# Performance work log

Hardware: AMD Instinct MI355X
Metric: run time of the kernel (lower is better)

The kernel has to match this reference:

```python
import jax, jax.numpy as jnp
import numpy as np

NUM_EXPERTS = 7
TRUNK_DIM = 64
HIDDEN = 64   # max(48, trunk_dim)
NUM_DEPTH_CLASSES = 3
BATCH = 262144


def setup_inputs() -> dict:
    key = jax.random.key(0)
    ks = jax.random.split(key, 8)
    trunk_feat = jax.random.normal(ks[0], (BATCH, TRUNK_DIM), dtype=jnp.float32)
    size_idx = jax.random.randint(ks[1], (BATCH,), 0, NUM_EXPERTS, dtype=jnp.int64)
    # Stacked expert MLP params: Linear(64,64) -> ReLU -> Linear(64,64) -> ReLU -> Linear(64,3)
    s1 = 1.0 / np.sqrt(TRUNK_DIM)
    s2 = 1.0 / np.sqrt(HIDDEN)
    W1 = jax.random.uniform(ks[2], (NUM_EXPERTS, TRUNK_DIM, HIDDEN), jnp.float32, -s1, s1)
    b1 = jax.random.uniform(ks[3], (NUM_EXPERTS, HIDDEN), jnp.float32, -s1, s1)
    W2 = jax.random.uniform(ks[4], (NUM_EXPERTS, HIDDEN, HIDDEN), jnp.float32, -s2, s2)
    b2 = jax.random.uniform(ks[5], (NUM_EXPERTS, HIDDEN), jnp.float32, -s2, s2)
    W3 = jax.random.uniform(ks[6], (NUM_EXPERTS, HIDDEN, NUM_DEPTH_CLASSES), jnp.float32, -s2, s2)
    b3 = jax.random.uniform(ks[7], (NUM_EXPERTS, NUM_DEPTH_CLASSES), jnp.float32, -s2, s2)
    return {"trunk_feat": trunk_feat, "size_idx": size_idx,
            "W1": W1, "b1": b1, "W2": W2, "b2": b2, "W3": W3, "b3": b3}


def _expert_mlp(x, W1, b1, W2, b2, W3, b3):
    # 3-layer MLP of one expert (dropout = identity in eval mode)
    h = jax.nn.relu(x @ W1 + b1)
    h = jax.nn.relu(h @ W2 + b2)
    return h @ W3 + b3  # [B, num_depth_classes]


def reference(trunk_feat, size_idx, W1, b1, W2, b2, W3, b3):
    # Hard routing (route_logits): rows with size_idx == e go through expert e;
    # expressed as masked accumulate so it is jit-friendly (no data-dependent shapes).
    B = trunk_feat.shape[0]
    logits = jnp.zeros((B, NUM_DEPTH_CLASSES), dtype=trunk_feat.dtype)
    for e in range(NUM_EXPERTS):  # fixed, small expert count
        le = _expert_mlp(trunk_feat, W1[e], b1[e], W2[e], b2[e], W3[e], b3[e])
        mask = (size_idx == e)[:, None]
        logits = logits + jnp.where(mask, le, jnp.zeros_like(le))
    probs = jax.nn.softmax(logits, axis=1)
    return logits, probs
```

## Files before the change

### kernel.cpp

```cpp
#include <hip/hip_runtime.h>
#include <stdint.h>

#define NE    7
#define DD    64
#define NDC   3
#define BLOCK 256
#define ROWS  256
#define NFRAG 18

typedef __fp16   half8 __attribute__((ext_vector_type(8)));
typedef float    f32x4 __attribute__((ext_vector_type(4)));
typedef uint32_t u32x4 __attribute__((ext_vector_type(4)));
typedef uint32_t u32x2 __attribute__((ext_vector_type(2)));
typedef __fp16   h2_t  __attribute__((ext_vector_type(2)));

__device__ __forceinline__ uint32_t pkrtz(float a, float b) {
  h2_t h = __builtin_amdgcn_cvt_pkrtz(a, b);
  return __builtin_bit_cast(uint32_t, h);
}
__device__ __forceinline__ f32x4 mfma16(u32x4 a, u32x4 b, f32x4 c) {
  return __builtin_amdgcn_mfma_f32_16x16x32_f16(
      __builtin_bit_cast(half8, a), __builtin_bit_cast(half8, b), c, 0, 0, 0);
}
__device__ __forceinline__ u32x4 relu_pack(f32x4 lo, f32x4 hi) {
  u32x4 t = { pkrtz(fmaxf(lo[0],0.f), fmaxf(lo[1],0.f)),
              pkrtz(fmaxf(lo[2],0.f), fmaxf(lo[3],0.f)),
              pkrtz(fmaxf(hi[0],0.f), fmaxf(hi[1],0.f)),
              pkrtz(fmaxf(hi[2],0.f), fmaxf(hi[3],0.f)) };
  return t;
}

__global__ __launch_bounds__(256) void pack_w2(
    const float* __restrict__ W1, const float* __restrict__ W2,
    const float* __restrict__ W3, uint32_t* __restrict__ ws) {
  __shared__ float wt[DD*DD];
  const int blk = blockIdx.x;
  const int e = blk >> 1, half = blk & 1;
  const float* Wsrc = (half ? W2 : W1) + (size_t)e*DD*DD;
  const float4* s4 = (const float4*)Wsrc;
  float4* d4 = (float4*)wt;
  #pragma unroll
  for (int i = 0; i < DD*DD/4/256; ++i)
    d4[i*256 + threadIdx.x] = s4[i*256 + threadIdx.x];
  __syncthreads();

  for (int idx = threadIdx.x; idx < 8*64; idx += 256) {
    const int fl = idx >> 6, l = idx & 63;
    const int nt = fl >> 1, ks = fl & 1;
    const int n  = nt*16 + (l & 15), g = l >> 4;
    uint32_t dst[4];
    #pragma unroll
    for (int d = 0; d < 4; ++d) {
      float v[2];
      #pragma unroll
      for (int h = 0; h < 2; ++h) {
        const int kk = 16*(d>>1) + 4*g + 2*(d&1) + h;
        v[h] = wt[(32*ks + kk)*DD + n];
      }
      dst[d] = pkrtz(v[0], v[1]);
    }
    uint32_t* p = ws + ((size_t)(e*NFRAG + half*8 + fl)*64 + l)*4;
    p[0]=dst[0]; p[1]=dst[1]; p[2]=dst[2]; p[3]=dst[3];
  }
  if (half == 0) {
    const float* Wl2 = W3 + (size_t)e*DD*NDC;
    for (int idx = threadIdx.x; idx < 2*64; idx += 256) {
      const int ks = idx >> 6, l = idx & 63;
      const int n  = l & 15, g = l >> 4;
      uint32_t dst[4];
      #pragma unroll
      for (int d = 0; d < 4; ++d) {
        float v[2];
        #pragma unroll
        for (int h = 0; h < 2; ++h) {
          const int kk = 16*(d>>1) + 4*g + 2*(d&1) + h;
          v[h] = (n < NDC) ? Wl2[(32*ks + kk)*NDC + n] : 0.0f;
        }
        dst[d] = pkrtz(v[0], v[1]);
      }
      uint32_t* p = ws + ((size_t)(e*NFRAG + 16 + ks)*64 + l)*4;
      p[0]=dst[0]; p[1]=dst[1]; p[2]=dst[2]; p[3]=dst[3];
    }
  }
}

__global__ __launch_bounds__(BLOCK, 3) void fused(
    const float* __restrict__ X, const int* __restrict__ S,
    const u32x4* __restrict__ wf,
    const float* __restrict__ b1, const float* __restrict__ b2,
    const float* __restrict__ b3,
    float* __restrict__ out, int B)
{
  __shared__ uint32_t pk[ROWS*32];
  __shared__ uint16_t srt[ROWS];
  __shared__ int wcnt[4][NE], woff[4][NE], cnt[NE];

  const int tid  = threadIdx.x;
  const int wv   = tid >> 6, lane = tid & 63;
  const int r15  = lane & 15, g = lane >> 4;
  const int base = blockIdx.x * ROWS;

  const int e_i = S[base + tid];

  u32x4 af[NFRAG];
  {
    const u32x4* wse = wf + (size_t)wv*NFRAG*64;
    #pragma unroll
    for (int f = 0; f < NFRAG; ++f) af[f] = wse[f*64 + lane];
  }

  {
    const float4* Xb = (const float4*)(X + (size_t)base * DD);
    #pragma unroll
    for (int it = 0; it < 16; ++it) {
      const int i = it*BLOCK + tid;
      const int r = i >> 4, q = i & 15;
      const float4 v = Xb[i];
      const int slotq = 4*(q >> 3) + (q & 3);
      const int hq    = (q >> 2) & 1;
      u32x2 w2 = { pkrtz(v.x, v.y), pkrtz(v.z, v.w) };
      *(u32x2*)&pk[r*32 + ((slotq ^ (r & 7)) << 2) + hq*2] = w2;
    }
  }

  int myprefix = 0;
  {
    unsigned long long mk[NE];
    #pragma unroll
    for (int q2 = 0; q2 < NE; ++q2) mk[q2] = __ballot(e_i == q2);
    #pragma unroll
    for (int q2 = 0; q2 < NE; ++q2)
      if (e_i == q2) myprefix = __popcll(mk[q2] & ((1ull << lane) - 1ull));
    if (lane < NE) wcnt[wv][lane] = __popcll(mk[lane]);
  }
  __syncthreads();

  if (wv == 0) {
    const int i = lane;
    int v = (i < 4*NE) ? wcnt[i & 3][i >> 2] : 0;
    int incl = v;
    #pragma unroll
    for (int d2 = 1; d2 < 32; d2 <<= 1) {
      const int t2 = __shfl_up(incl, d2, 64);
      if (lane >= d2) incl += t2;
    }
    const int excl = incl - v;
    if (i < 4*NE) woff[i & 3][i >> 2] = excl;
    const int incl3 = __shfl(incl, 4*lane + 3, 64);
    const int excl0 = __shfl(excl, 4*lane,     64);
    if (i < NE) cnt[i] = incl3 - excl0;
  }
  __syncthreads();

  srt[woff[wv][e_i] + myprefix] = (uint16_t)tid;
  __syncthreads();

  auto run_expert = [&](int e, const u32x4 (&A)[NFRAG]) {
    const int cn    = cnt[e];
    const int sbase = woff[0][e];
    const float4 bv1[4] = { *(const float4*)(b1 + e*DD +  0 + 4*g),
                            *(const float4*)(b1 + e*DD + 16 + 4*g),
                            *(const float4*)(b1 + e*DD + 32 + 4*g),
                            *(const float4*)(b1 + e*DD + 48 + 4*g) };
    const float4 bv2[4] = { *(const float4*)(b2 + e*DD +  0 + 4*g),
                            *(const float4*)(b2 + e*DD + 16 + 4*g),
                            *(const float4*)(b2 + e*DD + 32 + 4*g),
                            *(const float4*)(b2 + e*DD + 48 + 4*g) };
    const float bb0 = b3[e*NDC+0], bb1 = b3[e*NDC+1], bb2 = b3[e*NDC+2];

    for (int r0 = 0; r0 < cn; r0 += 16) {
      const int m  = cn - r0;
      const int lr = srt[sbase + r0 + min(r15, m - 1)];

      const u32x4 xf0 = *(const u32x4*)&pk[lr*32 + (((    g) ^ (lr & 7)) << 2)];
      const u32x4 xf1 = *(const u32x4*)&pk[lr*32 + (((4 + g) ^ (lr & 7)) << 2)];

      f32x4 c[4];
      #pragma unroll
      for (int nt = 0; nt < 4; ++nt) {
        f32x4 acc = { bv1[nt].x, bv1[nt].y, bv1[nt].z, bv1[nt].w };
        acc = mfma16(A[nt*2 + 0], xf0, acc);
        acc = mfma16(A[nt*2 + 1], xf1, acc);
        c[nt] = acc;
      }
      const u32x4 h0 = relu_pack(c[0], c[1]);
      const u32x4 h1 = relu_pack(c[2], c[3]);

      #pragma unroll
      for (int nt = 0; nt < 4; ++nt) {
        f32x4 acc = { bv2[nt].x, bv2[nt].y, bv2[nt].z, bv2[nt].w };
        acc = mfma16(A[8 + nt*2 + 0], h0, acc);
        acc = mfma16(A[8 + nt*2 + 1], h1, acc);
        c[nt] = acc;
      }
      const u32x4 t0 = relu_pack(c[0], c[1]);
      const u32x4 t1 = relu_pack(c[2], c[3]);

      f32x4 acc = { bb0, bb1, bb2, 0.f };
      acc = mfma16(A[16], t0, acc);
      acc = mfma16(A[17], t1, acc);

      if (g == 0 && r15 < m) {
        const int row = base + lr;
        const float l0 = acc[0], l1 = acc[1], l2 = acc[2];
        const float mx  = fmaxf(l0, fmaxf(l1, l2));
        const float p0  = __expf(l0 - mx);
        const float p1  = __expf(l1 - mx);
        const float p2  = __expf(l2 - mx);
        const float inv = 1.0f / (p0 + p1 + p2);
        float* o = out + (size_t)row*3;
        o[0] = l0; o[1] = l1; o[2] = l2;
        float* pr = out + (size_t)B*3 + (size_t)row*3;
        pr[0] = p0*inv; pr[1] = p1*inv; pr[2] = p2*inv;
      }
    }
  };

  run_expert(wv, af);

  if (wv < 3) {
    const int e2 = wv + 4;
    const u32x4* wse2 = wf + (size_t)e2*NFRAG*64;
    #pragma unroll
    for (int f = 0; f < NFRAG; ++f) af[f] = wse2[f*64 + lane];
    run_expert(e2, af);
  }
}

extern "C" void kernel_launch(void* const* d_in, const int* in_sizes, int n_in,
                              void* d_out, int out_size, void* d_ws, size_t ws_size,
                              hipStream_t stream)
{
  const float* X  = (const float*)d_in[0];
  const int*   S  = (const int*)d_in[1];
  const float* W1 = (const float*)d_in[2];
  const float* B1 = (const float*)d_in[3];
  const float* W2 = (const float*)d_in[4];
  const float* B2 = (const float*)d_in[5];
  const float* W3 = (const float*)d_in[6];
  const float* B3 = (const float*)d_in[7];
  float* out = (float*)d_out;
  uint32_t* ws = (uint32_t*)d_ws;

  const int B = in_sizes[0] / DD;

  pack_w2<<<NE*2, 256, 0, stream>>>(W1, W2, W3, ws);
  fused<<<B / ROWS, BLOCK, 0, stream>>>(X, S, (const u32x4*)ws,
                                        B1, B2, B3, out, B);
}
```

Measured before the change: 29.65 us.

## Use one wavefront per expert with 448-thread blocks

```diff
diff --git a/kernel.cpp b/kernel.cpp
--- a/kernel.cpp
+++ b/kernel.cpp
@@ -4,7 +4,7 @@
 #define NE    7
 #define DD    64
 #define NDC   3
-#define BLOCK 256
+#define BLOCK 448
 #define ROWS  256
 #define NFRAG 18
 
@@ -84,7 +84,7 @@
   }
 }
 
-__global__ __launch_bounds__(BLOCK, 3) void fused(
+__global__ __launch_bounds__(BLOCK, 2) void fused(
     const float* __restrict__ X, const int* __restrict__ S,
     const u32x4* __restrict__ wf,
     const float* __restrict__ b1, const float* __restrict__ b2,
@@ -99,21 +99,21 @@
   const int wv   = tid >> 6, lane = tid & 63;
   const int r15  = lane & 15, g = lane >> 4;
   const int base = blockIdx.x * ROWS;
-
-  const int e_i = S[base + tid];
+  const int e    = wv;
+
+  int e_i = 0;
+  if (wv < 4) e_i = S[base + tid];
 
   u32x4 af[NFRAG];
   {
-    const u32x4* wse = wf + (size_t)wv*NFRAG*64;
+    const u32x4* wse = wf + (size_t)e*NFRAG*64;
     #pragma unroll
     for (int f = 0; f < NFRAG; ++f) af[f] = wse[f*64 + lane];
   }
 
   {
     const float4* Xb = (const float4*)(X + (size_t)base * DD);
-    #pragma unroll
-    for (int it = 0; it < 16; ++it) {
-      const int i = it*BLOCK + tid;
+    for (int i = tid; i < ROWS*16; i += BLOCK) {
       const int r = i >> 4, q = i & 15;
       const float4 v = Xb[i];
       const int slotq = 4*(q >> 3) + (q & 3);
@@ -124,7 +124,7 @@
   }
 
   int myprefix = 0;
-  {
+  if (wv < 4) {
     unsigned long long mk[NE];
     #pragma unroll
     for (int q2 = 0; q2 < NE; ++q2) mk[q2] = __ballot(e_i == q2);
@@ -152,10 +152,10 @@
   }
   __syncthreads();
 
-  srt[woff[wv][e_i] + myprefix] = (uint16_t)tid;
-  __syncthreads();
-
-  auto run_expert = [&](int e, const u32x4 (&A)[NFRAG]) {
+  if (wv < 4) srt[woff[wv][e_i] + myprefix] = (uint16_t)tid;
+  __syncthreads();
+
+  {
     const int cn    = cnt[e];
     const int sbase = woff[0][e];
     const float4 bv1[4] = { *(const float4*)(b1 + e*DD +  0 + 4*g),
@@ -179,8 +179,8 @@
       #pragma unroll
       for (int nt = 0; nt < 4; ++nt) {
         f32x4 acc = { bv1[nt].x, bv1[nt].y, bv1[nt].z, bv1[nt].w };
-        acc = mfma16(A[nt*2 + 0], xf0, acc);
-        acc = mfma16(A[nt*2 + 1], xf1, acc);
+        acc = mfma16(af[nt*2 + 0], xf0, acc);
+        acc = mfma16(af[nt*2 + 1], xf1, acc);
         c[nt] = acc;
       }
       const u32x4 h0 = relu_pack(c[0], c[1]);
@@ -189,16 +189,16 @@
       #pragma unroll
       for (int nt = 0; nt < 4; ++nt) {
         f32x4 acc = { bv2[nt].x, bv2[nt].y, bv2[nt].z, bv2[nt].w };
-        acc = mfma16(A[8 + nt*2 + 0], h0, acc);
-        acc = mfma16(A[8 + nt*2 + 1], h1, acc);
+        acc = mfma16(af[8 + nt*2 + 0], h0, acc);
+        acc = mfma16(af[8 + nt*2 + 1], h1, acc);
         c[nt] = acc;
       }
       const u32x4 t0 = relu_pack(c[0], c[1]);
       const u32x4 t1 = relu_pack(c[2], c[3]);
 
       f32x4 acc = { bb0, bb1, bb2, 0.f };
-      acc = mfma16(A[16], t0, acc);
-      acc = mfma16(A[17], t1, acc);
+      acc = mfma16(af[16], t0, acc);
+      acc = mfma16(af[17], t1, acc);
 
       if (g == 0 && r15 < m) {
         const int row = base + lr;
@@ -214,16 +214,6 @@
         pr[0] = p0*inv; pr[1] = p1*inv; pr[2] = p2*inv;
       }
     }
-  };
-
-  run_expert(wv, af);
-
-  if (wv < 3) {
-    const int e2 = wv + 4;
-    const u32x4* wse2 = wf + (size_t)e2*NFRAG*64;
-    #pragma unroll
-    for (int f = 0; f < NFRAG; ++f) af[f] = wse2[f*64 + lane];
-    run_expert(e2, af);
   }
 }
 
```

After: 38.47 us. 1.3x slower.
